# Kernel optimization log

Hardware: AMD Instinct MI355X
Metric: run time of the kernel (lower is better)

## Reference

```python
import jax, jax.numpy as jnp
import numpy as np

WSIZE = 8
HEADS = 6
CYC_SHIFT = True


def _relative_index(w):
    # same math as SelfAttention._getRelativeIndex
    coords = np.stack(np.meshgrid(np.arange(w), np.arange(w), indexing='ij'))
    coords = coords.reshape(2, -1)                      # [2, w*w]
    rel = coords[:, :, None] - coords[:, None, :]       # [2, N, N]
    rel = rel.copy()
    rel[0] += w - 1
    rel[0] *= 2 * w - 1
    rel[1] += w - 1
    return (rel[0] + rel[1]).reshape(-1)                # [N*N]


def _shift_mask(H, W, w):
    # same math as CycShftWndwPartition._mask
    part = np.zeros((H, W), dtype=np.float32)
    slices = [slice(0, -w), slice(-w, -w // 2), slice(-w // 2, None)]
    idx = 0
    for hs in slices:
        for ws_ in slices:
            part[hs, ws_] = idx
            idx += 1
    part = part.reshape(H // w, w, W // w, w).transpose(0, 2, 1, 3).reshape(-1, w * w)
    diff = part[:, None, :] - part[:, :, None]          # [nW, N, N]
    return np.where(diff != 0, -100.0, 0.0).astype(np.float32)


def setup_inputs() -> dict:
    key = jax.random.key(0)
    k0, k1, k2, k3, k4 = jax.random.split(key, 5)
    B, H, W, C = 4, 384, 384, 60
    return {
        'cvrt_img': jax.random.normal(k0, (B, H, W, C), dtype=jnp.float32),
        'qkv_w': jax.random.normal(k1, (C, 3 * C), dtype=jnp.float32) * 0.05,
        'bias_matrix': jax.random.normal(k2, ((2 * WSIZE - 1) ** 2, HEADS), dtype=jnp.float32) * 0.02,
        'proj_w': jax.random.normal(k3, (C, C), dtype=jnp.float32) * 0.05,
        'proj_b': jax.random.normal(k4, (C,), dtype=jnp.float32) * 0.02,
    }


def reference(cvrt_img, qkv_w, bias_matrix, proj_w, proj_b):
    B, H, W, C = cvrt_img.shape
    w = WSIZE
    N = w * w
    d = C // HEADS
    nWh, nWw = H // w, W // w
    WNum = nWh * nWw

    # cyclic shift + window partition
    if CYC_SHIFT:
        x = jnp.roll(cvrt_img, shift=(-(w // 2), -(w // 2)), axis=(1, 2))
        mask = jnp.asarray(_shift_mask(H, W, w))        # [WNum, N, N]
    else:
        x = cvrt_img
        mask = jnp.zeros((WNum, N, N), dtype=cvrt_img.dtype)
    windows = x.reshape(B, nWh, w, nWw, w, C).transpose(0, 1, 3, 2, 4, 5)
    windows = windows.reshape(B * WNum, N, C)

    # windowed multi-head self-attention
    qkv = (windows @ qkv_w).reshape(B * WNum, N, 3, HEADS, d)
    qkv = qkv.transpose(2, 0, 3, 1, 4)                  # [3, Bw, H, N, d]
    q, k, v = qkv[0], qkv[1], qkv[2]
    attn = jnp.einsum('bhnd,bhmd->bhnm', q, k) / (d ** 0.5)

    rel_idx = jnp.asarray(_relative_index(w))
    bias = bias_matrix[rel_idx].reshape(N, N, HEADS).transpose(2, 0, 1)  # [H, N, N]
    attn = attn + bias[None]

    attn = attn.reshape(B, WNum, HEADS, N, N) + mask[None, :, None]
    attn = jax.nn.softmax(attn.reshape(B * WNum, HEADS, N, N), axis=-1)

    out = jnp.einsum('bhnm,bhmd->bhnd', attn, v)        # [Bw, H, N, d]
    out = out.transpose(0, 2, 1, 3).reshape(B * WNum, N, C)
    new_windows = out @ proj_w + proj_b

    # un-partition + reverse cyclic shift
    y = new_windows.reshape(B, nWh, nWw, w, w, C).transpose(0, 1, 3, 2, 4, 5)
    y = y.reshape(B, H, W, C)
    if CYC_SHIFT:
        y = jnp.roll(y, shift=(w // 2, w // 2), axis=(1, 2))
    return y
```

## Files before the change

kernel.cpp:

```cpp
#include <hip/hip_runtime.h>
#include <hip/hip_bf16.h>

#define IMG    384
#define CDIM   60
#define NWIN   48
#define WNUM   (NWIN * NWIN)

typedef short  bf16x8 __attribute__((ext_vector_type(8)));
typedef float  f32x4  __attribute__((ext_vector_type(4)));
union Frag { int4 i4; bf16x8 b8; };

#define MFMA(a, b, c) __builtin_amdgcn_mfma_f32_16x16x32_bf16((a), (b), (c), 0, 0, 0)

#define WS_QKVF  0
#define WS_VF    24576
#define WS_PROJF 36864
#define WS_BIASF 45056

#define SCALE_L2E (0.31622776601683794f * 1.4426950408889634f)
#define MASK_L2E  144.26950408889634f
#define LOG2E     1.4426950408889634f

__device__ __forceinline__ unsigned short f2bf(float f) {
    unsigned int u = __float_as_uint(f);
    unsigned int r = u + 0x7fffu + ((u >> 16) & 1u);
    return (unsigned short)(r >> 16);
}
__device__ __forceinline__ unsigned int pk2bf(float a, float b) {
    union { __hip_bfloat162 h; unsigned int u; } c;
    c.h = __float22bfloat162_rn(float2{a, b});
    return c.u;
}
__device__ __forceinline__ int regionOf(int x) {
    return (x < IMG - 8) ? 0 : ((x < IMG - 4) ? 1 : 2);
}
__device__ __forceinline__ int swz(int row, int byteoff) {
    return (row * 128 + byteoff) ^ ((row & 7) << 4);
}
__device__ __forceinline__ int4 qk_frag(const unsigned short* buf, int tok, int h, int g) {
    if (g == 0) return *(const int4*)((const char*)buf + swz(tok, h * 16));
    if (g == 1) {
        int v = *(const int*)((const char*)buf + swz(tok, 96 + h * 4));
        return int4{v, 0, 0, 0};
    }
    return int4{0, 0, 0, 0};
}

template<int MC>
__device__ __forceinline__ void attn_group(
    int h, int m0, int l15, int g, int dl, bool boundary, int wh, int ww,
    const unsigned short* qall, const unsigned short* kall,
    const unsigned short* vall, unsigned short* osb,
    char* slab, int prow, const float* biasf)
{
    Frag kb[4], va[2], qa[MC];
    #pragma unroll
    for (int n = 0; n < 4; ++n)
        kb[n].i4 = qk_frag(kall, n * 16 + l15, h, g);
    int vrow = (l15 < 10) ? h * 10 + l15 : 60;
    #pragma unroll
    for (int ks = 0; ks < 2; ++ks)
        va[ks].i4 = *(const int4*)((const char*)vall + swz(vrow, ks * 64 + g * 16));
    #pragma unroll
    for (int mm = 0; mm < MC; ++mm)
        qa[mm].i4 = qk_frag(qall, (m0 + mm) * 16 + l15, h, g);

    f32x4 scur[4], snxt[4];
    #pragma unroll
    for (int n = 0; n < 4; ++n) {
        f32x4 zz = {0.f, 0.f, 0.f, 0.f};
        scur[n] = MFMA(kb[n].b8, qa[0].b8, zz);
    }

    #pragma unroll
    for (int mm = 0; mm < MC; ++mm) {
        int i_tok = (m0 + mm) * 16 + l15;

        if (mm + 1 < MC) {
            #pragma unroll
            for (int n = 0; n < 4; ++n) {
                f32x4 zz = {0.f, 0.f, 0.f, 0.f};
                snxt[n] = MFMA(kb[n].b8, qa[mm + 1].b8, zz);
            }
        }

        const float* bp = biasf + ((h << 6) + i_tok) * 64;
        float p[4][4];
        #pragma unroll
        for (int n = 0; n < 4; ++n) {
            float4 bb = *(const float4*)(bp + n * 16 + (g << 2));
            p[n][0] = fmaf(scur[n][0], SCALE_L2E, bb.x);
            p[n][1] = fmaf(scur[n][1], SCALE_L2E, bb.y);
            p[n][2] = fmaf(scur[n][2], SCALE_L2E, bb.z);
            p[n][3] = fmaf(scur[n][3], SCALE_L2E, bb.w);
        }
        if (boundary) {
            int pi = regionOf(wh * 8 + (i_tok >> 3)) * 3 + regionOf(ww * 8 + (i_tok & 7));
            #pragma unroll
            for (int n = 0; n < 4; ++n)
                #pragma unroll
                for (int jj = 0; jj < 4; ++jj) {
                    int j = n * 16 + g * 4 + jj;
                    int pj = regionOf(wh * 8 + (j >> 3)) * 3 + regionOf(ww * 8 + (j & 7));
                    if (pi != pj) p[n][jj] -= MASK_L2E;
                }
        }
        unsigned w0[4], w1[4];
        #pragma unroll
        for (int n = 0; n < 4; ++n) {
            float e0 = __builtin_exp2f(p[n][0]);
            float e1 = __builtin_exp2f(p[n][1]);
            float e2 = __builtin_exp2f(p[n][2]);
            float e3 = __builtin_exp2f(p[n][3]);
            w0[n] = pk2bf(e0, e1);
            w1[n] = pk2bf(e2, e3);
        }
        f32x4 pv = {0.f, 0.f, 0.f, 0.f};
        *(int2*)(slab + swz(prow, 0 * 32 + g * 8)) = make_int2(w0[0], w1[0]);
        *(int2*)(slab + swz(prow, 1 * 32 + g * 8)) = make_int2(w0[1], w1[1]);
        {
            Frag pf;
            pf.i4 = *(const int4*)(slab + swz(prow, g * 16));
            pv = MFMA(va[0].b8, pf.b8, pv);
        }
        *(int2*)(slab + swz(prow, 0 * 32 + g * 8)) = make_int2(w0[2], w1[2]);
        *(int2*)(slab + swz(prow, 1 * 32 + g * 8)) = make_int2(w0[3], w1[3]);
        {
            Frag pf;
            pf.i4 = *(const int4*)(slab + swz(prow, g * 16));
            pv = MFMA(va[1].b8, pf.b8, pv);
        }
        float denom = __int_as_float(__builtin_amdgcn_ds_bpermute(dl, __float_as_int(pv[2])));
        float rinv  = __builtin_amdgcn_rcpf(denom);

        unsigned q01 = pk2bf(pv[0] * rinv, pv[1] * rinv);
        unsigned q23 = pk2bf(pv[2] * rinv, pv[3] * rinv);
        if (g < 2) {
            *(unsigned*)((char*)osb + swz(i_tok, h * 20 + g * 8 + 0)) = q01;
            *(unsigned*)((char*)osb + swz(i_tok, h * 20 + g * 8 + 4)) = q23;
        } else if (g == 2) {
            *(unsigned*)((char*)osb + swz(i_tok, h * 20 + 16)) = q01;
        }

        if (mm + 1 < MC) {
            #pragma unroll
            for (int n = 0; n < 4; ++n) scur[n] = snxt[n];
        }
    }
}

__global__ void swin_prep(const float* __restrict__ qw,
                          const float* __restrict__ pw,
                          const float* __restrict__ bias,
                          unsigned char* __restrict__ ws)
{
    int t = blockIdx.x * 256 + threadIdx.x;
    if (t < 1536) {
        int lane = t & 63, f = t >> 6;
        int mt = f >> 1, ks = f & 1;
        int h = mt >> 1, type = mt & 1;
        int d = lane & 15, g8 = lane >> 4;
        unsigned short v8[8];
        #pragma unroll
        for (int jj = 0; jj < 8; ++jj) {
            int c = ks * 32 + g8 * 8 + jj;
            v8[jj] = f2bf((d < 10 && c < 60) ? qw[c * 180 + type * 60 + h * 10 + d] : 0.f);
        }
        int4 p;
        p.x = v8[0] | (v8[1] << 16);  p.y = v8[2] | (v8[3] << 16);
        p.z = v8[4] | (v8[5] << 16);  p.w = v8[6] | (v8[7] << 16);
        *(int4*)(ws + WS_QKVF + t * 16) = p;
    } else if (t < 2304) {
        int t2 = t - 1536;
        int lane = t2 & 63, f = t2 >> 6;
        int h = f >> 1, ks = f & 1;
        int d = lane & 15, g8 = lane >> 4;
        unsigned short v8[8];
        #pragma unroll
        for (int jj = 0; jj < 8; ++jj) {
            int c = ks * 32 + g8 * 8 + jj;
            v8[jj] = f2bf((d < 10 && c < 60) ? qw[c * 180 + 120 + h * 10 + d] : 0.f);
        }
        int4 p;
        p.x = v8[0] | (v8[1] << 16);  p.y = v8[2] | (v8[3] << 16);
        p.z = v8[4] | (v8[5] << 16);  p.w = v8[6] | (v8[7] << 16);
        *(int4*)(ws + WS_VF + t2 * 16) = p;
    } else if (t < 2816) {
        int t2 = t - 2304;
        int lane = t2 & 63, fq = t2 >> 6;
        int m = fq >> 1, ks = fq & 1;
        int c = m * 16 + (lane & 15);
        int g8 = lane >> 4;
        unsigned short v8[8];
        #pragma unroll
        for (int jj = 0; jj < 8; ++jj) {
            int cc = ks * 32 + g8 * 8 + jj;
            v8[jj] = f2bf((c < 60 && cc < 60) ? pw[cc * 60 + c] : 0.f);
        }
        int4 p;
        p.x = v8[0] | (v8[1] << 16);  p.y = v8[2] | (v8[3] << 16);
        p.z = v8[4] | (v8[5] << 16);  p.w = v8[6] | (v8[7] << 16);
        *(int4*)(ws + WS_PROJF + t2 * 16) = p;
    } else if (t < 2816 + 24576) {
        int idx = t - 2816;
        int h = idx >> 12, r = idx & 4095;
        int i = r >> 6, j = r & 63;
        int yi = i >> 3, xi = i & 7, yj = j >> 3, xj = j & 7;
        int ridx = (yi - yj + 7) * 15 + (xi - xj + 7);
        ((float*)(ws + WS_BIASF))[h * 4096 + i * 64 + j] = bias[ridx * 6 + h] * LOG2E;
    }
}

__global__ __launch_bounds__(256, 4)
void swin_mfma(const float* __restrict__ img,
               const float* __restrict__ pbias,
               const unsigned char* __restrict__ ws,
               float* __restrict__ out)
{
    __shared__ __align__(16) unsigned short uni [64 * 64];
    __shared__ __align__(16) unsigned short qall[64 * 64];
    __shared__ __align__(16) unsigned short kall[64 * 64];
    __shared__ __align__(16) unsigned short vall[61 * 64];
    __shared__ __align__(16) unsigned short osb [64 * 64];

    const int tid  = threadIdx.x;
    const int lane = tid & 63;
    const int wid  = __builtin_amdgcn_readfirstlane(tid >> 6);
    const int l15  = lane & 15;
    const int g    = lane >> 4;
    const int dl   = (32 + l15) << 2;

    const int bid = blockIdx.x;
    const int b   = bid / WNUM;
    const int wi  = bid - b * WNUM;
    const int wh  = wi / NWIN;
    const int ww  = wi - wh * NWIN;
    const bool boundary = (wh == NWIN - 1) || (ww == NWIN - 1);

    {
        int tok = lane;
        int yi = tok >> 3, xi = tok & 7;
        int sh = wh * 8 + yi + 4; if (sh >= IMG) sh -= IMG;
        int sw = ww * 8 + xi + 4; if (sw >= IMG) sw -= IMG;
        const float* src = img + ((size_t)(b * IMG + sh) * IMG + sw) * CDIM;
        #pragma unroll
        for (int it = 0; it < 4; ++it) {
            int cg = wid + it * 4;
            if (cg < 15) {
                float4 v = *(const float4*)(src + cg * 4);
                *(int2*)((char*)uni + swz(tok, cg * 8)) =
                    make_int2(pk2bf(v.x, v.y), pk2bf(v.z, v.w));
            } else {
                *(int2*)((char*)uni + swz(tok, 120)) = make_int2(0, 0);
            }
        }
    }
    if (tid < 128) {
        int row = tid >> 1, half = tid & 1;
        *(unsigned int*)((char*)osb + swz(row, 120 + half * 4)) = 0u;
    }
    if (tid < 32) {
        *(unsigned int*)((char*)vall + swz(60, tid * 4)) = 0x3F803F80u;
    }
    __syncthreads();

    {
        Frag xb[4][2];
        #pragma unroll
        for (int n = 0; n < 4; ++n)
            #pragma unroll
            for (int ks = 0; ks < 2; ++ks)
                xb[n][ks].i4 = *(const int4*)((const char*)uni + swz(n * 16 + l15, ks * 64 + g * 16));

        const int4* wsq = (const int4*)(ws + WS_QKVF);
        #pragma unroll
        for (int kk = 0; kk < 3; ++kk) {
            int mt = wid + kk * 4;
            int h = mt >> 1, type = mt & 1;
            Frag a0, a1;
            a0.i4 = wsq[(mt * 2 + 0) * 64 + lane];
            a1.i4 = wsq[(mt * 2 + 1) * 64 + lane];
            unsigned short* dst = type ? kall : qall;
            #pragma unroll
            for (int n = 0; n < 4; ++n) {
                f32x4 acc = {0.f, 0.f, 0.f, 0.f};
                acc = MFMA(a0.b8, xb[n][0].b8, acc);
                acc = MFMA(a1.b8, xb[n][1].b8, acc);
                int tok = n * 16 + l15;
                unsigned pk01 = pk2bf(acc[0], acc[1]);
                unsigned pk23 = pk2bf(acc[2], acc[3]);
                if (g < 2)
                    *(int2*)((char*)dst + swz(tok, h * 16 + g * 8)) = make_int2(pk01, pk23);
                else if (g == 2)
                    *(unsigned*)((char*)dst + swz(tok, 96 + h * 4)) = pk01;
            }
        }
        const int4* wsv = (const int4*)(ws + WS_VF);
        int nv = (wid < 2) ? 2 : 1;
        #pragma unroll 1
        for (int kk = 0; kk < nv; ++kk) {
            int hv = wid + kk * 4;
            Frag b0, b1;
            b0.i4 = wsv[(hv * 2 + 0) * 64 + lane];
            b1.i4 = wsv[(hv * 2 + 1) * 64 + lane];
            #pragma unroll
            for (int n = 0; n < 4; ++n) {
                f32x4 acc = {0.f, 0.f, 0.f, 0.f};
                acc = MFMA(xb[n][0].b8, b0.b8, acc);
                acc = MFMA(xb[n][1].b8, b1.b8, acc);
                if (l15 < 10) {
                    *(int2*)((char*)vall + swz(hv * 10 + l15, n * 32 + g * 8)) =
                        make_int2(pk2bf(acc[0], acc[1]), pk2bf(acc[2], acc[3]));
                }
            }
        }
    }
    __syncthreads();

    {
        char* slab = (char*)uni;
        const int prow = wid * 16 + l15;
        const float* biasf = (const float*)(ws + WS_BIASF);
        const int h0 = wid + (wid >> 1);

        if ((wid & 1) == 0) {
            attn_group<4>(h0,     0, l15, g, dl, boundary, wh, ww, qall, kall, vall, osb, slab, prow, biasf);
            attn_group<2>(h0 + 1, 0, l15, g, dl, boundary, wh, ww, qall, kall, vall, osb, slab, prow, biasf);
        } else {
            attn_group<2>(h0,     2, l15, g, dl, boundary, wh, ww, qall, kall, vall, osb, slab, prow, biasf);
            attn_group<4>(h0 + 1, 0, l15, g, dl, boundary, wh, ww, qall, kall, vall, osb, slab, prow, biasf);
        }
    }
    __syncthreads();

    {
        const int4* wsp = (const int4*)(ws + WS_PROJF);
        Frag a0, a1;
        a0.i4 = wsp[(wid * 2 + 0) * 64 + lane];
        a1.i4 = wsp[(wid * 2 + 1) * 64 + lane];
        int c0 = wid * 16 + g * 4;
        float4 pbv = (c0 < 60) ? *(const float4*)&pbias[c0] : float4{0.f, 0.f, 0.f, 0.f};
        #pragma unroll
        for (int n = 0; n < 4; ++n) {
            Frag b0, b1;
            b0.i4 = *(const int4*)((const char*)osb + swz(n * 16 + l15, g * 16));
            b1.i4 = *(const int4*)((const char*)osb + swz(n * 16 + l15, 64 + g * 16));
            f32x4 acc = {0.f, 0.f, 0.f, 0.f};
            acc = MFMA(a0.b8, b0.b8, acc);
            acc = MFMA(a1.b8, b1.b8, acc);
            if (c0 < 60) {
                int tok = n * 16 + l15;
                int yi = tok >> 3, xi = tok & 7;
                int sh = wh * 8 + yi + 4; if (sh >= IMG) sh -= IMG;
                int sw = ww * 8 + xi + 4; if (sw >= IMG) sw -= IMG;
                float4 o = {acc[0] + pbv.x, acc[1] + pbv.y, acc[2] + pbv.z, acc[3] + pbv.w};
                *(float4*)&out[((b * IMG + sh) * IMG + sw) * CDIM + c0] = o;
            }
        }
    }
}

extern "C" void kernel_launch(void* const* d_in, const int* in_sizes, int n_in,
                              void* d_out, int out_size, void* d_ws, size_t ws_size,
                              hipStream_t stream) {
    const float* img  = (const float*)d_in[0];
    const float* qw   = (const float*)d_in[1];
    const float* bias = (const float*)d_in[2];
    const float* pw   = (const float*)d_in[3];
    const float* pb   = (const float*)d_in[4];
    float* out = (float*)d_out;

    swin_prep<<<107, 256, 0, stream>>>(qw, pw, bias, (unsigned char*)d_ws);
    swin_mfma<<<4 * WNUM, 256, 0, stream>>>(img, pb,
                                            (const unsigned char*)d_ws, out);
}
```

Baseline: 180.0 us.

## Fold softmax scale into Q weights, preload bias as MFMA accumulator, alias output buffer

Folds the attention scale and log2e factor into the Q projection weights at prep time. The relative-position bias is stored in MFMA fragment order so it can be loaded directly as the accumulator input of the QK^T MFMA, which removes the per-element FMA. The separate osb LDS buffer is dropped: K fragments for both heads are loaded into registers up front, then a barrier lets kall be reused as the attention output buffer. This cuts LDS footprint, which may raise occupancy, but it adds a barrier and holds more K fragments in registers while removing the QK software pipelining.

```diff
diff --git a/kernel.cpp b/kernel.cpp
--- a/kernel.cpp
+++ b/kernel.cpp
@@ -15,7 +15,7 @@
 #define WS_QKVF  0
 #define WS_VF    24576
 #define WS_PROJF 36864
-#define WS_BIASF 45056
+#define WS_BIASC 45056
 
 #define SCALE_L2E (0.31622776601683794f * 1.4426950408889634f)
 #define MASK_L2E  144.26950408889634f
@@ -48,51 +48,32 @@
 
 template<int MC>
 __device__ __forceinline__ void attn_group(
-    int h, int m0, int l15, int g, int dl, bool boundary, int wh, int ww,
-    const unsigned short* qall, const unsigned short* kall,
-    const unsigned short* vall, unsigned short* osb,
-    char* slab, int prow, const float* biasf)
+    int h, int m0, const Frag (&kb)[4],
+    int lane, int l15, int g, int dl, bool boundary, int wh, int ww,
+    const unsigned short* qall, const unsigned short* vall,
+    unsigned short* osb,
+    char* slab, int prow, const float4* biasC)
 {
-    Frag kb[4], va[2], qa[MC];
-    #pragma unroll
-    for (int n = 0; n < 4; ++n)
-        kb[n].i4 = qk_frag(kall, n * 16 + l15, h, g);
+    Frag va[2];
     int vrow = (l15 < 10) ? h * 10 + l15 : 60;
     #pragma unroll
     for (int ks = 0; ks < 2; ++ks)
         va[ks].i4 = *(const int4*)((const char*)vall + swz(vrow, ks * 64 + g * 16));
-    #pragma unroll
-    for (int mm = 0; mm < MC; ++mm)
-        qa[mm].i4 = qk_frag(qall, (m0 + mm) * 16 + l15, h, g);
-
-    f32x4 scur[4], snxt[4];
-    #pragma unroll
-    for (int n = 0; n < 4; ++n) {
-        f32x4 zz = {0.f, 0.f, 0.f, 0.f};
-        scur[n] = MFMA(kb[n].b8, qa[0].b8, zz);
-    }
 
     #pragma unroll
     for (int mm = 0; mm < MC; ++mm) {
-        int i_tok = (m0 + mm) * 16 + l15;
-
-        if (mm + 1 < MC) {
-            #pragma unroll
-            for (int n = 0; n < 4; ++n) {
-                f32x4 zz = {0.f, 0.f, 0.f, 0.f};
-                snxt[n] = MFMA(kb[n].b8, qa[mm + 1].b8, zz);
-            }
-        }
-
-        const float* bp = biasf + ((h << 6) + i_tok) * 64;
-        float p[4][4];
+        int m = m0 + mm;
+        int i_tok = m * 16 + l15;
+        Frag qa;
+        qa.i4 = qk_frag(qall, i_tok, h, g);
+
+        const float4* bc = biasC + (h * 16 + m * 4) * 64 + lane;
+        f32x4 sacc[4];
         #pragma unroll
         for (int n = 0; n < 4; ++n) {
-            float4 bb = *(const float4*)(bp + n * 16 + (g << 2));
-            p[n][0] = fmaf(scur[n][0], SCALE_L2E, bb.x);
-            p[n][1] = fmaf(scur[n][1], SCALE_L2E, bb.y);
-            p[n][2] = fmaf(scur[n][2], SCALE_L2E, bb.z);
-            p[n][3] = fmaf(scur[n][3], SCALE_L2E, bb.w);
+            float4 bb = bc[n * 64];
+            f32x4 ci = {bb.x, bb.y, bb.z, bb.w};
+            sacc[n] = MFMA(kb[n].b8, qa.b8, ci);
         }
         if (boundary) {
             int pi = regionOf(wh * 8 + (i_tok >> 3)) * 3 + regionOf(ww * 8 + (i_tok & 7));
@@ -102,16 +83,16 @@
                 for (int jj = 0; jj < 4; ++jj) {
                     int j = n * 16 + g * 4 + jj;
                     int pj = regionOf(wh * 8 + (j >> 3)) * 3 + regionOf(ww * 8 + (j & 7));
-                    if (pi != pj) p[n][jj] -= MASK_L2E;
+                    if (pi != pj) sacc[n][jj] -= MASK_L2E;
                 }
         }
         unsigned w0[4], w1[4];
         #pragma unroll
         for (int n = 0; n < 4; ++n) {
-            float e0 = __builtin_exp2f(p[n][0]);
-            float e1 = __builtin_exp2f(p[n][1]);
-            float e2 = __builtin_exp2f(p[n][2]);
-            float e3 = __builtin_exp2f(p[n][3]);
+            float e0 = __builtin_exp2f(sacc[n][0]);
+            float e1 = __builtin_exp2f(sacc[n][1]);
+            float e2 = __builtin_exp2f(sacc[n][2]);
+            float e3 = __builtin_exp2f(sacc[n][3]);
             w0[n] = pk2bf(e0, e1);
             w1[n] = pk2bf(e2, e3);
         }
@@ -140,11 +121,6 @@
             *(unsigned*)((char*)osb + swz(i_tok, h * 20 + g * 8 + 4)) = q23;
         } else if (g == 2) {
             *(unsigned*)((char*)osb + swz(i_tok, h * 20 + 16)) = q01;
-        }
-
-        if (mm + 1 < MC) {
-            #pragma unroll
-            for (int n = 0; n < 4; ++n) scur[n] = snxt[n];
         }
     }
 }
@@ -164,7 +140,9 @@
         #pragma unroll
         for (int jj = 0; jj < 8; ++jj) {
             int c = ks * 32 + g8 * 8 + jj;
-            v8[jj] = f2bf((d < 10 && c < 60) ? qw[c * 180 + type * 60 + h * 10 + d] : 0.f);
+            float wv = (d < 10 && c < 60) ? qw[c * 180 + type * 60 + h * 10 + d] : 0.f;
+            if (type == 0) wv *= SCALE_L2E;
+            v8[jj] = f2bf(wv);
         }
         int4 p;
         p.x = v8[0] | (v8[1] << 16);  p.y = v8[2] | (v8[3] << 16);
@@ -203,11 +181,17 @@
         *(int4*)(ws + WS_PROJF + t2 * 16) = p;
     } else if (t < 2816 + 24576) {
         int idx = t - 2816;
-        int h = idx >> 12, r = idx & 4095;
-        int i = r >> 6, j = r & 63;
+        int h = idx >> 12;
+        int r = idx & 4095;
+        int m = r >> 10;
+        int n = (r >> 8) & 3;
+        int lane = (r >> 2) & 63;
+        int jj = r & 3;
+        int i = m * 16 + (lane & 15);
+        int j = n * 16 + (lane >> 4) * 4 + jj;
         int yi = i >> 3, xi = i & 7, yj = j >> 3, xj = j & 7;
         int ridx = (yi - yj + 7) * 15 + (xi - xj + 7);
-        ((float*)(ws + WS_BIASF))[h * 4096 + i * 64 + j] = bias[ridx * 6 + h] * LOG2E;
+        ((float*)(ws + WS_BIASC))[idx] = bias[ridx * 6 + h] * LOG2E;
     }
 }
 
@@ -221,7 +205,6 @@
     __shared__ __align__(16) unsigned short qall[64 * 64];
     __shared__ __align__(16) unsigned short kall[64 * 64];
     __shared__ __align__(16) unsigned short vall[61 * 64];
-    __shared__ __align__(16) unsigned short osb [64 * 64];
 
     const int tid  = threadIdx.x;
     const int lane = tid & 63;
@@ -257,7 +240,7 @@
     }
     if (tid < 128) {
         int row = tid >> 1, half = tid & 1;
-        *(unsigned int*)((char*)osb + swz(row, 120 + half * 4)) = 0u;
+        *(unsigned int*)((char*)kall + swz(row, 120 + half * 4)) = 0u;
     }
     if (tid < 32) {
         *(unsigned int*)((char*)vall + swz(60, tid * 4)) = 0x3F803F80u;
@@ -320,15 +303,28 @@
     {
         char* slab = (char*)uni;
         const int prow = wid * 16 + l15;
-        const float* biasf = (const float*)(ws + WS_BIASF);
+        const float4* biasC = (const float4*)(ws + WS_BIASC);
         const int h0 = wid + (wid >> 1);
+        const int h1 = h0 + 1;
+
+        Frag kb0[4], kb1[4];
+        #pragma unroll
+        for (int n = 0; n < 4; ++n) {
+            kb0[n].i4 = qk_frag(kall, n * 16 + l15, h0, g);
+            kb1[n].i4 = qk_frag(kall, n * 16 + l15, h1, g);
+        }
+        __syncthreads();
 
         if ((wid & 1) == 0) {
-            attn_group<4>(h0,     0, l15, g, dl, boundary, wh, ww, qall, kall, vall, osb, slab, prow, biasf);
-            attn_group<2>(h0 + 1, 0, l15, g, dl, boundary, wh, ww, qall, kall, vall, osb, slab, prow, biasf);
+            attn_group<4>(h0, 0, kb0, lane, l15, g, dl, boundary, wh, ww,
+                          qall, vall, kall, slab, prow, biasC);
+            attn_group<2>(h1, 0, kb1, lane, l15, g, dl, boundary, wh, ww,
+                          qall, vall, kall, slab, prow, biasC);
         } else {
-            attn_group<2>(h0,     2, l15, g, dl, boundary, wh, ww, qall, kall, vall, osb, slab, prow, biasf);
-            attn_group<4>(h0 + 1, 0, l15, g, dl, boundary, wh, ww, qall, kall, vall, osb, slab, prow, biasf);
+            attn_group<2>(h0, 2, kb0, lane, l15, g, dl, boundary, wh, ww,
+                          qall, vall, kall, slab, prow, biasC);
+            attn_group<4>(h1, 0, kb1, lane, l15, g, dl, boundary, wh, ww,
+                          qall, vall, kall, slab, prow, biasC);
         }
     }
     __syncthreads();
@@ -343,8 +339,8 @@
         #pragma unroll
         for (int n = 0; n < 4; ++n) {
             Frag b0, b1;
-            b0.i4 = *(const int4*)((const char*)osb + swz(n * 16 + l15, g * 16));
-            b1.i4 = *(const int4*)((const char*)osb + swz(n * 16 + l15, 64 + g * 16));
+            b0.i4 = *(const int4*)((const char*)kall + swz(n * 16 + l15, g * 16));
+            b1.i4 = *(const int4*)((const char*)kall + swz(n * 16 + l15, 64 + g * 16));
             f32x4 acc = {0.f, 0.f, 0.f, 0.f};
             acc = MFMA(a0.b8, b0.b8, acc);
             acc = MFMA(a1.b8, b1.b8, acc);
```

New measurement: 163.5 us. 9.2% less time.
